# Optimization experiments

Hardware: AMD Instinct MI355X
Metric: run time of the kernel (lower is better)

## Reference

```python
import jax, jax.numpy as jnp
import numpy as np


def setup_inputs() -> dict:
    key = jax.random.key(0)
    image = jax.random.uniform(key, (16, 3, 1024, 1024), dtype=jnp.float32)
    return {"image": image, "patch_size": 5}


def reference(image, patch_size):
    # Local (population) variance over a patch_size x patch_size sliding window
    # with reflect padding. Var = E[X^2] - E[X]^2, identical math to the
    # unfold-based mean((x - mean)^2) in the torch source.
    pad = patch_size // 2
    xp = jnp.pad(image, ((0, 0), (0, 0), (pad, pad), (pad, pad)), mode="reflect")
    n = jnp.asarray(patch_size * patch_size, dtype=image.dtype)

    def box_mean(x):
        # windowed sum via reduce_window, VALID -> output back to [B,C,H,W]
        s = jax.lax.reduce_window(
            x, jnp.asarray(0.0, x.dtype), jax.lax.add,
            window_dimensions=(1, 1, patch_size, patch_size),
            window_strides=(1, 1, 1, 1), padding="VALID")
        return s / n

    m = box_mean(xp)
    m2 = box_mean(xp * xp)
    return m2 - m * m
```

## Files before the change

kernel.cpp:

```cpp
#include <hip/hip_runtime.h>


constexpr int NT = 256;

__global__ __launch_bounds__(NT, 4)
void lvar5x5_reg_kernel(const float* __restrict__ in, float* __restrict__ out,
                        int H, int W) {
    const int tx = threadIdx.x & 63;
    const int ty = threadIdx.x >> 6;
    const int c0 = blockIdx.x * 256 + tx * 4;
    const int r0 = blockIdx.y * 32 + ty * 8;
    const size_t plane = (size_t)H * W;
    const float* __restrict__ img = in + (size_t)blockIdx.z * plane;
    float* __restrict__ o = out + (size_t)blockIdx.z * plane;

    const bool cL = (c0 == 0);
    const bool cR = (c0 == W - 4);
    const int a0 = cL ? 0 : c0 - 4;
    const int a2 = cR ? c0 : c0 + 4;

    float rh[5][4];
    float rq[5][4];
    float sh0 = 0.f, sh1 = 0.f, sh2 = 0.f, sh3 = 0.f;
    float sq0 = 0.f, sq1 = 0.f, sq2 = 0.f, sq3 = 0.f;

    const float inv = 1.0f / 25.0f;

#pragma unroll
    for (int i = 0; i < 12; ++i) {
        int gy = r0 - 2 + i;
        gy = (gy < 0) ? -gy : ((gy >= H) ? (2 * H - 2 - gy) : gy);
        const float* __restrict__ row = img + (size_t)gy * W;

        const float4 v0 = *reinterpret_cast<const float4*>(row + a0);
        const float4 v1 = *reinterpret_cast<const float4*>(row + c0);
        const float4 v2 = *reinterpret_cast<const float4*>(row + a2);

        const float x2 = v0.z;
        float       x3 = v0.w;
        const float x4 = v1.x, x5 = v1.y, x6 = v1.z, x7 = v1.w;
        float       x8 = v2.x;
        const float x9 = v2.y;
        if (cL) x3 = x5;
        if (cR) x8 = x6;

        const float h0 = x2 + x3 + x4 + x5 + x6;
        const float h1 = h0 - x2 + x7;
        const float h2 = h1 - x3 + x8;
        const float h3 = h2 - x4 + x9;

        const float y2 = x2 * x2, y3 = x3 * x3, y4 = x4 * x4, y5 = x5 * x5;
        const float y6 = x6 * x6, y7 = x7 * x7, y8 = x8 * x8, y9 = x9 * x9;
        const float q0 = y2 + y3 + y4 + y5 + y6;
        const float q1 = q0 - y2 + y7;
        const float q2 = q1 - y3 + y8;
        const float q3 = q2 - y4 + y9;

        const int s = i % 5;
        if (i >= 5) {
            sh0 -= rh[s][0]; sh1 -= rh[s][1]; sh2 -= rh[s][2]; sh3 -= rh[s][3];
            sq0 -= rq[s][0]; sq1 -= rq[s][1]; sq2 -= rq[s][2]; sq3 -= rq[s][3];
        }
        rh[s][0] = h0; rh[s][1] = h1; rh[s][2] = h2; rh[s][3] = h3;
        rq[s][0] = q0; rq[s][1] = q1; rq[s][2] = q2; rq[s][3] = q3;
        sh0 += h0; sh1 += h1; sh2 += h2; sh3 += h3;
        sq0 += q0; sq1 += q1; sq2 += q2; sq3 += q3;

        if (i >= 4) {
            float4 res;
            float m;
            m = sh0 * inv; res.x = fmaf(-m, m, sq0 * inv);
            m = sh1 * inv; res.y = fmaf(-m, m, sq1 * inv);
            m = sh2 * inv; res.z = fmaf(-m, m, sq2 * inv);
            m = sh3 * inv; res.w = fmaf(-m, m, sq3 * inv);
            *reinterpret_cast<float4*>(
                o + (size_t)(r0 + i - 4) * W + c0) = res;
        }
    }
}

extern "C" void kernel_launch(void* const* d_in, const int* in_sizes, int n_in,
                              void* d_out, int out_size, void* d_ws, size_t ws_size,
                              hipStream_t stream) {
    const float* image = (const float*)d_in[0];
    float* out = (float*)d_out;

    const int H = 1024, W = 1024;
    const int BC = out_size / (H * W);

    dim3 grid(W / 256, H / 32, BC);
    dim3 block(NT);
    lvar5x5_reg_kernel<<<grid, block, 0, stream>>>(image, out, H, W);
}
```

Measured before the change: 335.1 us.

## Widen per-thread tile to 8 columns x 16 rows with nontemporal stores

Each thread now produces an 8-wide by 16-tall output strip instead of 4x8, reading only 2-column halos per side rather than full float4 neighbours. This cuts redundant halo loads horizontally and the 4-row vertical halo overhead per output row. Stores use nontemporal hints to avoid polluting cache. The larger per-thread state raises register pressure (launch bounds lowered to 3) and reduces total thread count and parallelism.

```diff
diff --git a/kernel.cpp b/kernel.cpp
--- a/kernel.cpp
+++ b/kernel.cpp
@@ -2,79 +2,84 @@
 
 
 constexpr int NT = 256;
+typedef float v4f __attribute__((ext_vector_type(4)));
 
-__global__ __launch_bounds__(NT, 4)
-void lvar5x5_reg_kernel(const float* __restrict__ in, float* __restrict__ out,
-                        int H, int W) {
-    const int tx = threadIdx.x & 63;
-    const int ty = threadIdx.x >> 6;
-    const int c0 = blockIdx.x * 256 + tx * 4;
-    const int r0 = blockIdx.y * 32 + ty * 8;
+__global__ __launch_bounds__(NT, 3)
+void lvar5x5_reg8_kernel(const float* __restrict__ in, float* __restrict__ out,
+                         int H, int W) {
+    const int tx = threadIdx.x & 31;
+    const int ty = threadIdx.x >> 5;
+    const int c0 = blockIdx.x * 256 + tx * 8;
+    const int r0 = blockIdx.y * 128 + ty * 16;
     const size_t plane = (size_t)H * W;
     const float* __restrict__ img = in + (size_t)blockIdx.z * plane;
     float* __restrict__ o = out + (size_t)blockIdx.z * plane;
 
     const bool cL = (c0 == 0);
-    const bool cR = (c0 == W - 4);
-    const int a0 = cL ? 0 : c0 - 4;
-    const int a2 = cR ? c0 : c0 + 4;
+    const bool cR = (c0 == W - 8);
+    const int aL = cL ? c0 : c0 - 2;
+    const int aR = cR ? c0 + 4 : c0 + 8;
 
-    float rh[5][4];
-    float rq[5][4];
-    float sh0 = 0.f, sh1 = 0.f, sh2 = 0.f, sh3 = 0.f;
-    float sq0 = 0.f, sq1 = 0.f, sq2 = 0.f, sq3 = 0.f;
+    float rh[5][8];
+    float rq[5][8];
+    float sh[8], sq[8];
+#pragma unroll
+    for (int j = 0; j < 8; ++j) { sh[j] = 0.f; sq[j] = 0.f; }
 
     const float inv = 1.0f / 25.0f;
 
 #pragma unroll
-    for (int i = 0; i < 12; ++i) {
+    for (int i = 0; i < 20; ++i) {
         int gy = r0 - 2 + i;
         gy = (gy < 0) ? -gy : ((gy >= H) ? (2 * H - 2 - gy) : gy);
         const float* __restrict__ row = img + (size_t)gy * W;
 
-        const float4 v0 = *reinterpret_cast<const float4*>(row + a0);
-        const float4 v1 = *reinterpret_cast<const float4*>(row + c0);
-        const float4 v2 = *reinterpret_cast<const float4*>(row + a2);
+        const float2 L = *reinterpret_cast<const float2*>(row + aL);
+        const float4 A = *reinterpret_cast<const float4*>(row + c0);
+        const float4 B = *reinterpret_cast<const float4*>(row + c0 + 4);
+        const float2 R = *reinterpret_cast<const float2*>(row + aR);
 
-        const float x2 = v0.z;
-        float       x3 = v0.w;
-        const float x4 = v1.x, x5 = v1.y, x6 = v1.z, x7 = v1.w;
-        float       x8 = v2.x;
-        const float x9 = v2.y;
-        if (cL) x3 = x5;
-        if (cR) x8 = x6;
+        float xv[12];
+        xv[0] = L.x; xv[1] = L.y;
+        xv[2] = A.x; xv[3] = A.y; xv[4] = A.z; xv[5] = A.w;
+        xv[6] = B.x; xv[7] = B.y; xv[8] = B.z; xv[9] = B.w;
+        xv[10] = R.x; xv[11] = R.y;
+        if (cL) { xv[0] = A.z; xv[1] = A.y; }
+        if (cR) { xv[10] = B.z; xv[11] = B.y; }
 
-        const float h0 = x2 + x3 + x4 + x5 + x6;
-        const float h1 = h0 - x2 + x7;
-        const float h2 = h1 - x3 + x8;
-        const float h3 = h2 - x4 + x9;
+        float yv[12];
+#pragma unroll
+        for (int k = 0; k < 12; ++k) yv[k] = xv[k] * xv[k];
 
-        const float y2 = x2 * x2, y3 = x3 * x3, y4 = x4 * x4, y5 = x5 * x5;
-        const float y6 = x6 * x6, y7 = x7 * x7, y8 = x8 * x8, y9 = x9 * x9;
-        const float q0 = y2 + y3 + y4 + y5 + y6;
-        const float q1 = q0 - y2 + y7;
-        const float q2 = q1 - y3 + y8;
-        const float q3 = q2 - y4 + y9;
+        float h[8], q[8];
+        h[0] = xv[0] + xv[1] + xv[2] + xv[3] + xv[4];
+        q[0] = yv[0] + yv[1] + yv[2] + yv[3] + yv[4];
+#pragma unroll
+        for (int j = 1; j < 8; ++j) {
+            h[j] = h[j - 1] - xv[j - 1] + xv[j + 4];
+            q[j] = q[j - 1] - yv[j - 1] + yv[j + 4];
+        }
 
         const int s = i % 5;
-        if (i >= 5) {
-            sh0 -= rh[s][0]; sh1 -= rh[s][1]; sh2 -= rh[s][2]; sh3 -= rh[s][3];
-            sq0 -= rq[s][0]; sq1 -= rq[s][1]; sq2 -= rq[s][2]; sq3 -= rq[s][3];
+#pragma unroll
+        for (int j = 0; j < 8; ++j) {
+            if (i >= 5) { sh[j] -= rh[s][j]; sq[j] -= rq[s][j]; }
+            rh[s][j] = h[j]; rq[s][j] = q[j];
+            sh[j] += h[j];   sq[j] += q[j];
         }
-        rh[s][0] = h0; rh[s][1] = h1; rh[s][2] = h2; rh[s][3] = h3;
-        rq[s][0] = q0; rq[s][1] = q1; rq[s][2] = q2; rq[s][3] = q3;
-        sh0 += h0; sh1 += h1; sh2 += h2; sh3 += h3;
-        sq0 += q0; sq1 += q1; sq2 += q2; sq3 += q3;
 
         if (i >= 4) {
-            float4 res;
-            float m;
-            m = sh0 * inv; res.x = fmaf(-m, m, sq0 * inv);
-            m = sh1 * inv; res.y = fmaf(-m, m, sq1 * inv);
-            m = sh2 * inv; res.z = fmaf(-m, m, sq2 * inv);
-            m = sh3 * inv; res.w = fmaf(-m, m, sq3 * inv);
-            *reinterpret_cast<float4*>(
-                o + (size_t)(r0 + i - 4) * W + c0) = res;
+            float res[8];
+#pragma unroll
+            for (int j = 0; j < 8; ++j) {
+                const float m = sh[j] * inv;
+                res[j] = fmaf(-m, m, sq[j] * inv);
+            }
+            float* dst = o + (size_t)(r0 + i - 4) * W + c0;
+            v4f lo = { res[0], res[1], res[2], res[3] };
+            v4f hi = { res[4], res[5], res[6], res[7] };
+            __builtin_nontemporal_store(lo, (v4f*)dst);
+            __builtin_nontemporal_store(hi, (v4f*)(dst + 4));
         }
     }
 }
@@ -88,7 +93,7 @@
     const int H = 1024, W = 1024;
     const int BC = out_size / (H * W);
 
-    dim3 grid(W / 256, H / 32, BC);
+    dim3 grid(W / 256, H / 128, BC);
     dim3 block(NT);
-    lvar5x5_reg_kernel<<<grid, block, 0, stream>>>(image, out, H, W);
+    lvar5x5_reg8_kernel<<<grid, block, 0, stream>>>(image, out, H, W);
 }
```

Result: slower. 366.2 us (+9.3%).
